# Kernel tuning notes

Measured on AMD Instinct MI355X. Metric: run time of the kernel, lower is better.

The kernel has to match this reference:

```python
import jax, jax.numpy as jnp
import numpy as np
from jax import lax

DN = ('NHWC', 'HWIO', 'NHWC')


def setup_inputs() -> dict:
    key = jax.random.key(0)
    k1, k2, k3, k4, k5, k6 = jax.random.split(key, 6)
    B = 1024
    vals = jax.random.normal(k1, (B, 64, 64, 1), dtype=jnp.float32)
    active = (jax.random.uniform(k2, (B, 64, 64, 1)) < 0.1).astype(jnp.float32)
    x = vals * active
    W1 = jax.random.normal(k3, (3, 3, 1, 64), dtype=jnp.float32) * 0.1
    b1 = jax.random.normal(k4, (64,), dtype=jnp.float32) * 0.1
    W2 = jax.random.normal(k5, (3, 3, 64, 32), dtype=jnp.float32) * 0.05
    b2 = jax.random.normal(k6, (32,), dtype=jnp.float32) * 0.05
    return {"x": x, "W1": W1, "b1": b1, "W2": W2, "b2": b2}


def reference(x, W1, b1, W2, b2):
    # x: [B, 64, 64, 1] NHWC (spconv from_dense layout); active sites = nonzero pixels
    m0 = (jnp.abs(x).max(axis=-1, keepdims=True) > 0).astype(x.dtype)  # [B,64,64,1]
    # SparseConv2d(1,64,3,stride=1, pad=0): output indices = any active input in 3x3 window
    m1 = lax.reduce_window(m0, jnp.array(0, x.dtype), lax.max,
                           (1, 3, 3, 1), (1, 1, 1, 1), 'VALID')  # [B,62,62,1]
    y = lax.conv_general_dilated(x, W1, (1, 1), 'VALID', dimension_numbers=DN)
    y = (y + b1) * m1  # bias only at active output sites; [B,62,62,64]
    # SparseInverseConv2d(64,32,3): transposed conv restricted to the ORIGINAL
    # active index set (indice_key='cp0'), i.e. output only where m0 is active.
    z = lax.conv_transpose(y, W2, (1, 1), 'VALID', dimension_numbers=DN)  # [B,64,64,32]
    z = (z + b2) * m0
    # SparseConvTensor.dense() returns NCHW
    return jnp.transpose(z, (0, 3, 1, 2))
```

## Files before the change

### kernel.cpp

```cpp
#include <hip/hip_runtime.h>

#define BDIM 256
#define KC_STRIDE 28
#define CASE_STRIDE (32 * KC_STRIDE)
#define SP 1032

typedef float floatx4 __attribute__((ext_vector_type(4)));

__device__ __forceinline__ int casef(int p) {
  return ((unsigned)(p - 2) < 60u) ? 2 : (p < 2 ? p : p - 59);
}

__global__ __launch_bounds__(BDIM) void prep_kernel(
    const float* __restrict__ W1, const float* __restrict__ b1,
    const float* __restrict__ W2, const float* __restrict__ b2,
    float* __restrict__ ws) {
  __shared__ float Mlds[9 * 9 * 32];
  __shared__ float BvL[9 * 32];
  const int tid = threadIdx.x;
  const int co = tid & 31;
  for (int tap = tid >> 5; tap < 9; tap += 8) {
    float acc[9] = {0.f, 0.f, 0.f, 0.f, 0.f, 0.f, 0.f, 0.f, 0.f};
    float accB = 0.f;
    for (int ci = 0; ci < 64; ++ci) {
      float w2 = W2[(tap * 64 + ci) * 32 + co];
      accB = fmaf(b1[ci], w2, accB);
#pragma unroll
      for (int e = 0; e < 9; ++e) acc[e] = fmaf(W1[e * 64 + ci], w2, acc[e]);
    }
#pragma unroll
    for (int e = 0; e < 9; ++e) Mlds[(tap * 9 + e) * 32 + co] = acc[e];
    BvL[tap * 32 + co] = accB;
  }
  __syncthreads();

  const int a = blockIdx.x / 5, c = blockIdx.x % 5;
  const int dmask[5] = {4, 6, 7, 3, 1};
  const int Da = dmask[a], Dc = dmask[c];
  for (int t = tid; t < CASE_STRIDE; t += BDIM) {
    int cc = t / KC_STRIDE, r = t % KC_STRIDE;
    float s = 0.f;
    if (r < 25) {
      int u = r / 5, v = r % 5;
      for (int di = 0; di < 3; ++di) {
        if (!((Da >> di) & 1)) continue;
        int ei = u - di;
        if ((unsigned)ei > 2u) continue;
        for (int dj = 0; dj < 3; ++dj) {
          if (!((Dc >> dj) & 1)) continue;
          int ej = v - dj;
          if ((unsigned)ej > 2u) continue;
          s += Mlds[((di * 3 + dj) * 9 + ei * 3 + ej) * 32 + cc];
        }
      }
    } else if (r == 25) {
      s = b2[cc];
      for (int di = 0; di < 3; ++di)
        if ((Da >> di) & 1)
          for (int dj = 0; dj < 3; ++dj)
            if ((Dc >> dj) & 1) s += BvL[(di * 3 + dj) * 32 + cc];
    }
    ws[blockIdx.x * CASE_STRIDE + t] = s;
  }
}

__global__ __launch_bounds__(BDIM) void main_kernel(
    const float* __restrict__ x, const float* __restrict__ ws,
    float* __restrict__ out) {
  const int bb = blockIdx.x;
  const int b = bb >> 1;
  const int r0 = (bb & 1) << 5;
  const int tid = threadIdx.x;
  const int lane = tid & 63;
  const int wave = tid >> 6;

  __shared__ __align__(16) float xp[36 * 68];
  __shared__ __align__(16) float S[8][SP];
  __shared__ __align__(16) float KiL[CASE_STRIDE];
  __shared__ unsigned long long Rm[32];
  __shared__ unsigned short aqi[2][224], aqb[2][64];
  __shared__ int nqi_sh[2], nqb_sh[2];

  if (tid < 2) { nqi_sh[tid] = 0; nqb_sh[tid] = 0; }
  float4* xp4 = reinterpret_cast<float4*>(xp);
  for (int i = tid; i < 612; i += BDIM) xp4[i] = make_float4(0.f, 0.f, 0.f, 0.f);
  for (int i = tid; i < CASE_STRIDE; i += BDIM) KiL[i] = ws[12 * CASE_STRIDE + i];
  __syncthreads();

  const float* xb = x + (size_t)b * 4096;
  for (int it = tid; it < 576; it += BDIM) {
    int i = it >> 4, c4 = (it & 15) << 2;
    int r = r0 - 2 + i;
    if ((unsigned)r < 64u) {
      float4 v = *reinterpret_cast<const float4*>(xb + r * 64 + c4);
      float2* d2 = reinterpret_cast<float2*>(&xp[i * 68 + 2 + c4]);
      d2[0] = make_float2(v.x, v.y);
      d2[1] = make_float2(v.z, v.w);
    }
  }
  __syncthreads();

  for (int k = wave; k < 32; k += 4) {
    int pred = (xp[(k + 2) * 68 + 2 + lane] != 0.0f);
    unsigned long long m = __ballot(pred);
    if (lane == 0) Rm[k] = m;
  }
  __syncthreads();

  for (int g = tid; g < 512; g += BDIM) {
    int k = g >> 4, q0 = (g & 15) << 2;
    unsigned bits = (unsigned)(Rm[k] >> q0) & 0xFu;
    if (!bits) continue;
    int h = k >> 4;
    int p = r0 + k;
    bool inter = ((unsigned)(p - 2) < 60u) && ((unsigned)(q0 - 4) <= 52u);
    if (inter) {
      aqi[h][atomicAdd(&nqi_sh[h], 1)] = (unsigned short)g;
    } else {
      aqb[h][atomicAdd(&nqb_sh[h], 1)] = (unsigned short)g;
    }
  }
  __syncthreads();

  const int ni0 = nqi_sh[0], ni1 = nqi_sh[1];
  const int nb0 = nqb_sh[0], nb1 = nqb_sh[1];
  float* outb = out + (size_t)b * (32 * 4096);

  for (int t = 0; t < 8; ++t) {
    const int cg = t >> 1, h = t & 1;
    const int ni = h ? ni1 : ni0;
    const int nb = h ? nb1 : nb0;
    for (int n = tid; n < ni * 4; n += BDIM) {
      int g = aqi[h][n >> 2];
      int co4 = n & 3;
      int co_lo = (cg << 3) + co4;
      int k = g >> 4, q0 = (g & 15) << 2;
      const float* Ka = &KiL[co_lo * KC_STRIDE];
      const float* Kb = &KiL[(co_lo + 4) * KC_STRIDE];
      float ba = Ka[25], bbv = Kb[25];
      float a0 = ba, a1 = ba, a2 = ba, a3 = ba;
      float b0 = bbv, b1 = bbv, b2 = bbv, b3 = bbv;
#pragma unroll
      for (int u = 0; u < 5; ++u) {
        const float* xr = &xp[(k + u) * 68 + q0];
        float4 xa = *reinterpret_cast<const float4*>(xr);
        float4 xc = *reinterpret_cast<const float4*>(xr + 4);
        float xv[8] = {xa.x, xa.y, xa.z, xa.w, xc.x, xc.y, xc.z, xc.w};
#pragma unroll
        for (int v = 0; v < 5; ++v) {
          float ka = Ka[u * 5 + v], kb = Kb[u * 5 + v];
          a0 = fmaf(xv[v], ka, a0);
          a1 = fmaf(xv[v + 1], ka, a1);
          a2 = fmaf(xv[v + 2], ka, a2);
          a3 = fmaf(xv[v + 3], ka, a3);
          b0 = fmaf(xv[v], kb, b0);
          b1 = fmaf(xv[v + 1], kb, b1);
          b2 = fmaf(xv[v + 2], kb, b2);
          b3 = fmaf(xv[v + 3], kb, b3);
        }
      }
      int so = ((k & 15) << 6) + q0;
      *reinterpret_cast<float4*>(&S[co4][so]) = make_float4(a0, a1, a2, a3);
      *reinterpret_cast<float4*>(&S[co4 + 4][so]) = make_float4(b0, b1, b2, b3);
    }
    for (int n = tid; n < nb * 8; n += BDIM) {
      int g = aqb[h][n >> 3];
      int cs = n & 7;
      int co = (cg << 3) + cs;
      int k = g >> 4, q0 = (g & 15) << 2;
      int p = r0 + k;
      int cp = casef(p);
      const float* K0 = ws + ((cp * 5 + casef(q0)) * 32 + co) * KC_STRIDE;
      const float* K1 = ws + ((cp * 5 + casef(q0 + 1)) * 32 + co) * KC_STRIDE;
      const float* K2 = ws + ((cp * 5 + casef(q0 + 2)) * 32 + co) * KC_STRIDE;
      const float* K3 = ws + ((cp * 5 + casef(q0 + 3)) * 32 + co) * KC_STRIDE;
      float z0 = K0[25], z1 = K1[25], z2 = K2[25], z3 = K3[25];
#pragma unroll
      for (int u = 0; u < 5; ++u) {
        const float* xr = &xp[(k + u) * 68 + q0];
        float4 xa = *reinterpret_cast<const float4*>(xr);
        float4 xc = *reinterpret_cast<const float4*>(xr + 4);
        float xv[8] = {xa.x, xa.y, xa.z, xa.w, xc.x, xc.y, xc.z, xc.w};
#pragma unroll
        for (int v = 0; v < 5; ++v) {
          int o = u * 5 + v;
          z0 = fmaf(xv[v], K0[o], z0);
          z1 = fmaf(xv[v + 1], K1[o], z1);
          z2 = fmaf(xv[v + 2], K2[o], z2);
          z3 = fmaf(xv[v + 3], K3[o], z3);
        }
      }
      *reinterpret_cast<float4*>(&S[cs][((k & 15) << 6) + q0]) =
          make_float4(z0, z1, z2, z3);
    }
    asm volatile("s_waitcnt lgkmcnt(0)" ::: "memory");
    __builtin_amdgcn_s_barrier();
    {
      int co_a = (cg << 3) + wave;
      int co_b = co_a + 4;
      float* dstA = outb + (((size_t)co_a) << 12) + ((r0 + (h << 4)) << 6);
      float* dstB = outb + (((size_t)co_b) << 12) + ((r0 + (h << 4)) << 6);
      const floatx4* SpA = reinterpret_cast<const floatx4*>(&S[wave][0]);
      const floatx4* SpB = reinterpret_cast<const floatx4*>(&S[wave + 4][0]);
#pragma unroll
      for (int i = 0; i < 4; ++i) {
        int f4 = (i << 6) + lane;
        int kk = f4 >> 4, q0 = (f4 & 15) << 2;
        unsigned bits = (unsigned)(Rm[(h << 4) + kk] >> q0) & 0xFu;
        floatx4 va = SpA[f4];
        floatx4 vb = SpB[f4];
        if (!(bits & 1u)) { va.x = 0.f; vb.x = 0.f; }
        if (!(bits & 2u)) { va.y = 0.f; vb.y = 0.f; }
        if (!(bits & 4u)) { va.z = 0.f; vb.z = 0.f; }
        if (!(bits & 8u)) { va.w = 0.f; vb.w = 0.f; }
        __builtin_nontemporal_store(va, reinterpret_cast<floatx4*>(dstA + (f4 << 2)));
        __builtin_nontemporal_store(vb, reinterpret_cast<floatx4*>(dstB + (f4 << 2)));
      }
    }
    asm volatile("s_waitcnt lgkmcnt(0)" ::: "memory");
    __builtin_amdgcn_s_barrier();
  }
}

extern "C" void kernel_launch(void* const* d_in, const int* in_sizes, int n_in,
                              void* d_out, int out_size, void* d_ws, size_t ws_size,
                              hipStream_t stream) {
  const float* x  = (const float*)d_in[0];
  const float* W1 = (const float*)d_in[1];
  const float* b1 = (const float*)d_in[2];
  const float* W2 = (const float*)d_in[3];
  const float* b2 = (const float*)d_in[4];
  float* out = (float*)d_out;
  float* ws  = (float*)d_ws;
  int B = in_sizes[0] / 4096;

  hipLaunchKernelGGL(prep_kernel, dim3(25), dim3(BDIM), 0, stream, W1, b1, W2, b2, ws);
  hipLaunchKernelGGL(main_kernel, dim3(2 * B), dim3(BDIM), 0, stream, x, ws, out);
}
```

Measured before the change: 136.0 us.

## Compute border outputs as interior kernel minus row/column/corner corrections from LDS

Border pixel groups no longer read per-case fused 5x5 kernels from global memory. They start from the interior kernel held in LDS and subtract precomputed row and column correction terms, then add corner terms back, with all tables staged in shared memory. A 26th prep block writes these correction tables. The aim is to remove scattered global loads in the border path, at the cost of extra LDS per block (about 24KB), which may lower occupancy, and extra FMAs for border pixels.

```diff
diff --git a/kernel.cpp b/kernel.cpp
--- a/kernel.cpp
+++ b/kernel.cpp
@@ -4,6 +4,13 @@
 #define KC_STRIDE 28
 #define CASE_STRIDE (32 * KC_STRIDE)
 #define SP 1032
+
+#define OFF_M 22400
+#define OFF_MR 24992
+#define OFF_MC 26432
+#define OFF_BVR 27872
+#define OFF_BVC 27968
+#define OFF_BV 28064
 
 typedef float floatx4 __attribute__((ext_vector_type(4)));
 
@@ -34,35 +41,93 @@
   }
   __syncthreads();
 
-  const int a = blockIdx.x / 5, c = blockIdx.x % 5;
-  const int dmask[5] = {4, 6, 7, 3, 1};
-  const int Da = dmask[a], Dc = dmask[c];
-  for (int t = tid; t < CASE_STRIDE; t += BDIM) {
-    int cc = t / KC_STRIDE, r = t % KC_STRIDE;
-    float s = 0.f;
-    if (r < 25) {
-      int u = r / 5, v = r % 5;
+  if (blockIdx.x < 25) {
+    const int a = blockIdx.x / 5, c = blockIdx.x % 5;
+    const int dmask[5] = {4, 6, 7, 3, 1};
+    const int Da = dmask[a], Dc = dmask[c];
+    for (int t = tid; t < CASE_STRIDE; t += BDIM) {
+      int cc = t / KC_STRIDE, r = t % KC_STRIDE;
+      float s = 0.f;
+      if (r < 25) {
+        int u = r / 5, v = r % 5;
+        for (int di = 0; di < 3; ++di) {
+          if (!((Da >> di) & 1)) continue;
+          int ei = u - di;
+          if ((unsigned)ei > 2u) continue;
+          for (int dj = 0; dj < 3; ++dj) {
+            if (!((Dc >> dj) & 1)) continue;
+            int ej = v - dj;
+            if ((unsigned)ej > 2u) continue;
+            s += Mlds[((di * 3 + dj) * 9 + ei * 3 + ej) * 32 + cc];
+          }
+        }
+      } else if (r == 25) {
+        s = b2[cc];
+        for (int di = 0; di < 3; ++di)
+          if ((Da >> di) & 1)
+            for (int dj = 0; dj < 3; ++dj)
+              if ((Dc >> dj) & 1) s += BvL[(di * 3 + dj) * 32 + cc];
+      }
+      ws[blockIdx.x * CASE_STRIDE + t] = s;
+    }
+  } else {
+    for (int t = tid; t < 2592; t += BDIM) ws[OFF_M + t] = Mlds[t];
+    for (int t = tid; t < 1440; t += BDIM) {
+      int di = t / 480, r = (t / 32) % 15, cc = t & 31;
+      int ei = r / 5, v = r % 5;
+      float s = 0.f;
+      for (int dj = 0; dj < 3; ++dj) {
+        int ej = v - dj;
+        if ((unsigned)ej <= 2u) s += Mlds[((di * 3 + dj) * 9 + ei * 3 + ej) * 32 + cc];
+      }
+      ws[OFF_MR + t] = s;
+    }
+    for (int t = tid; t < 1440; t += BDIM) {
+      int dj = t / 480, r = (t / 32) % 15, cc = t & 31;
+      int u = r / 3, ej = r % 3;
+      float s = 0.f;
       for (int di = 0; di < 3; ++di) {
-        if (!((Da >> di) & 1)) continue;
         int ei = u - di;
-        if ((unsigned)ei > 2u) continue;
-        for (int dj = 0; dj < 3; ++dj) {
-          if (!((Dc >> dj) & 1)) continue;
-          int ej = v - dj;
-          if ((unsigned)ej > 2u) continue;
-          s += Mlds[((di * 3 + dj) * 9 + ei * 3 + ej) * 32 + cc];
-        }
-      }
-    } else if (r == 25) {
-      s = b2[cc];
-      for (int di = 0; di < 3; ++di)
-        if ((Da >> di) & 1)
-          for (int dj = 0; dj < 3; ++dj)
-            if ((Dc >> dj) & 1) s += BvL[(di * 3 + dj) * 32 + cc];
-    }
-    ws[blockIdx.x * CASE_STRIDE + t] = s;
+        if ((unsigned)ei <= 2u) s += Mlds[((di * 3 + dj) * 9 + ei * 3 + ej) * 32 + cc];
+      }
+      ws[OFF_MC + t] = s;
+    }
+    for (int t = tid; t < 96; t += BDIM) {
+      int di = t >> 5, cc = t & 31;
+      float s = 0.f;
+      for (int dj = 0; dj < 3; ++dj) s += BvL[(di * 3 + dj) * 32 + cc];
+      ws[OFF_BVR + t] = s;
+    }
+    for (int t = tid; t < 96; t += BDIM) {
+      int dj = t >> 5, cc = t & 31;
+      float s = 0.f;
+      for (int di = 0; di < 3; ++di) s += BvL[(di * 3 + dj) * 32 + cc];
+      ws[OFF_BVC + t] = s;
+    }
+    for (int t = tid; t < 288; t += BDIM) ws[OFF_BV + t] = BvL[t];
   }
 }
+
+#define ROWCORR(DI)                                                            \
+  { float bv = BvRl[(DI)*32 + co]; z0 -= bv; z1 -= bv; z2 -= bv; z3 -= bv;     \
+    _Pragma("unroll") for (int ei = 0; ei < 3; ++ei)                           \
+    _Pragma("unroll") for (int v = 0; v < 5; ++v) {                            \
+      float m = MRl[((DI)*15 + ei*5 + v)*32 + co];                             \
+      z0 = fmaf(-xw[(DI)+ei][v], m, z0);   z1 = fmaf(-xw[(DI)+ei][v+1], m, z1);\
+      z2 = fmaf(-xw[(DI)+ei][v+2], m, z2); z3 = fmaf(-xw[(DI)+ei][v+3], m, z3);} }
+
+#define COLCORR(DJ, J, Z)                                                      \
+  { Z -= BvCl[(DJ)*32 + co];                                                   \
+    _Pragma("unroll") for (int u = 0; u < 5; ++u)                              \
+    _Pragma("unroll") for (int ej = 0; ej < 3; ++ej)                           \
+      Z = fmaf(-xw[u][(DJ)+ej+(J)], MCl[((DJ)*15 + u*3 + ej)*32 + co], Z); }
+
+#define CORNER(DI, DJ, J, Z)                                                   \
+  { Z += Bvl[((DI)*3+(DJ))*32 + co];                                           \
+    _Pragma("unroll") for (int ei = 0; ei < 3; ++ei)                           \
+    _Pragma("unroll") for (int ej = 0; ej < 3; ++ej)                           \
+      Z = fmaf(xw[(DI)+ei][(DJ)+ej+(J)],                                       \
+               Ml[(((DI)*3+(DJ))*9 + ei*3 + ej)*32 + co], Z); }
 
 __global__ __launch_bounds__(BDIM) void main_kernel(
     const float* __restrict__ x, const float* __restrict__ ws,
@@ -77,6 +142,8 @@
   __shared__ __align__(16) float xp[36 * 68];
   __shared__ __align__(16) float S[8][SP];
   __shared__ __align__(16) float KiL[CASE_STRIDE];
+  __shared__ float Ml[2592], MRl[1440], MCl[1440];
+  __shared__ float BvRl[96], BvCl[96], Bvl[288];
   __shared__ unsigned long long Rm[32];
   __shared__ unsigned short aqi[2][224], aqb[2][64];
   __shared__ int nqi_sh[2], nqb_sh[2];
@@ -85,6 +152,10 @@
   float4* xp4 = reinterpret_cast<float4*>(xp);
   for (int i = tid; i < 612; i += BDIM) xp4[i] = make_float4(0.f, 0.f, 0.f, 0.f);
   for (int i = tid; i < CASE_STRIDE; i += BDIM) KiL[i] = ws[12 * CASE_STRIDE + i];
+  for (int i = tid; i < 2592; i += BDIM) Ml[i] = ws[OFF_M + i];
+  for (int i = tid; i < 1440; i += BDIM) { MRl[i] = ws[OFF_MR + i]; MCl[i] = ws[OFF_MC + i]; }
+  if (tid < 96) { BvRl[tid] = ws[OFF_BVR + tid]; BvCl[tid] = ws[OFF_BVC + tid]; }
+  for (int i = tid; i < 288; i += BDIM) Bvl[i] = ws[OFF_BV + i];
   __syncthreads();
 
   const float* xb = x + (size_t)b * 4096;
@@ -169,26 +240,49 @@
       int co = (cg << 3) + cs;
       int k = g >> 4, q0 = (g & 15) << 2;
       int p = r0 + k;
-      int cp = casef(p);
-      const float* K0 = ws + ((cp * 5 + casef(q0)) * 32 + co) * KC_STRIDE;
-      const float* K1 = ws + ((cp * 5 + casef(q0 + 1)) * 32 + co) * KC_STRIDE;
-      const float* K2 = ws + ((cp * 5 + casef(q0 + 2)) * 32 + co) * KC_STRIDE;
-      const float* K3 = ws + ((cp * 5 + casef(q0 + 3)) * 32 + co) * KC_STRIDE;
-      float z0 = K0[25], z1 = K1[25], z2 = K2[25], z3 = K3[25];
+      float xw[5][8];
 #pragma unroll
       for (int u = 0; u < 5; ++u) {
         const float* xr = &xp[(k + u) * 68 + q0];
         float4 xa = *reinterpret_cast<const float4*>(xr);
         float4 xc = *reinterpret_cast<const float4*>(xr + 4);
-        float xv[8] = {xa.x, xa.y, xa.z, xa.w, xc.x, xc.y, xc.z, xc.w};
+        xw[u][0] = xa.x; xw[u][1] = xa.y; xw[u][2] = xa.z; xw[u][3] = xa.w;
+        xw[u][4] = xc.x; xw[u][5] = xc.y; xw[u][6] = xc.z; xw[u][7] = xc.w;
+      }
+      const float* Ki = &KiL[co * KC_STRIDE];
+      float bias = Ki[25];
+      float z0 = bias, z1 = bias, z2 = bias, z3 = bias;
+#pragma unroll
+      for (int u = 0; u < 5; ++u) {
 #pragma unroll
         for (int v = 0; v < 5; ++v) {
-          int o = u * 5 + v;
-          z0 = fmaf(xv[v], K0[o], z0);
-          z1 = fmaf(xv[v + 1], K1[o], z1);
-          z2 = fmaf(xv[v + 2], K2[o], z2);
-          z3 = fmaf(xv[v + 3], K3[o], z3);
+          float kv = Ki[u * 5 + v];
+          z0 = fmaf(xw[u][v], kv, z0);
+          z1 = fmaf(xw[u][v + 1], kv, z1);
+          z2 = fmaf(xw[u][v + 2], kv, z2);
+          z3 = fmaf(xw[u][v + 3], kv, z3);
         }
+      }
+      if (p == 0)       { ROWCORR(0) ROWCORR(1) }
+      else if (p == 1)  { ROWCORR(0) }
+      else if (p == 62) { ROWCORR(2) }
+      else if (p == 63) { ROWCORR(1) ROWCORR(2) }
+      if (q0 == 0) {
+        COLCORR(0, 0, z0) COLCORR(1, 0, z0) COLCORR(0, 1, z1)
+        if (p == 0)       { CORNER(0,0,0,z0) CORNER(0,1,0,z0) CORNER(0,0,1,z1)
+                            CORNER(1,0,0,z0) CORNER(1,1,0,z0) CORNER(1,0,1,z1) }
+        else if (p == 1)  { CORNER(0,0,0,z0) CORNER(0,1,0,z0) CORNER(0,0,1,z1) }
+        else if (p == 62) { CORNER(2,0,0,z0) CORNER(2,1,0,z0) CORNER(2,0,1,z1) }
+        else if (p == 63) { CORNER(1,0,0,z0) CORNER(1,1,0,z0) CORNER(1,0,1,z1)
+                            CORNER(2,0,0,z0) CORNER(2,1,0,z0) CORNER(2,0,1,z1) }
+      } else if (q0 == 60) {
+        COLCORR(2, 2, z2) COLCORR(1, 3, z3) COLCORR(2, 3, z3)
+        if (p == 0)       { CORNER(0,2,2,z2) CORNER(0,1,3,z3) CORNER(0,2,3,z3)
+                            CORNER(1,2,2,z2) CORNER(1,1,3,z3) CORNER(1,2,3,z3) }
+        else if (p == 1)  { CORNER(0,2,2,z2) CORNER(0,1,3,z3) CORNER(0,2,3,z3) }
+        else if (p == 62) { CORNER(2,2,2,z2) CORNER(2,1,3,z3) CORNER(2,2,3,z3) }
+        else if (p == 63) { CORNER(1,2,2,z2) CORNER(1,1,3,z3) CORNER(1,2,3,z3)
+                            CORNER(2,2,2,z2) CORNER(2,1,3,z3) CORNER(2,2,3,z3) }
       }
       *reinterpret_cast<float4*>(&S[cs][((k & 15) << 6) + q0]) =
           make_float4(z0, z1, z2, z3);
@@ -197,9 +291,8 @@
     __builtin_amdgcn_s_barrier();
     {
       int co_a = (cg << 3) + wave;
-      int co_b = co_a + 4;
       float* dstA = outb + (((size_t)co_a) << 12) + ((r0 + (h << 4)) << 6);
-      float* dstB = outb + (((size_t)co_b) << 12) + ((r0 + (h << 4)) << 6);
+      float* dstB = outb + (((size_t)(co_a + 4)) << 12) + ((r0 + (h << 4)) << 6);
       const floatx4* SpA = reinterpret_cast<const floatx4*>(&S[wave][0]);
       const floatx4* SpB = reinterpret_cast<const floatx4*>(&S[wave + 4][0]);
 #pragma unroll
@@ -234,6 +327,6 @@
   float* ws  = (float*)d_ws;
   int B = in_sizes[0] / 4096;
 
-  hipLaunchKernelGGL(prep_kernel, dim3(25), dim3(BDIM), 0, stream, W1, b1, W2, b2, ws);
+  hipLaunchKernelGGL(prep_kernel, dim3(26), dim3(BDIM), 0, stream, W1, b1, W2, b2, ws);
   hipLaunchKernelGGL(main_kernel, dim3(2 * B), dim3(BDIM), 0, stream, x, ws, out);
 }
```

Result: slower. 164.7 us (+21.2%).

## Process full 32-row tile per channel group and hold interior weights in registers

Applied to the files above, without the earlier changes.

The staging buffer S is doubled so each channel group handles all 32 rows at once, halving the outer loop from 8 to 4 iterations and cutting barrier count. The interior kernel weights are now loaded from global memory into per-thread register arrays once per channel group instead of being read from a shared-memory copy. This removes the LDS copy of the weights and the per-FMA LDS weight reads, at the cost of higher register pressure and nearly double the shared memory for S, which may reduce occupancy.

```diff
diff --git a/kernel.cpp b/kernel.cpp
--- a/kernel.cpp
+++ b/kernel.cpp
@@ -3,7 +3,7 @@
 #define BDIM 256
 #define KC_STRIDE 28
 #define CASE_STRIDE (32 * KC_STRIDE)
-#define SP 1032
+#define SP 2052
 
 typedef float floatx4 __attribute__((ext_vector_type(4)));
 
@@ -76,15 +76,13 @@
 
   __shared__ __align__(16) float xp[36 * 68];
   __shared__ __align__(16) float S[8][SP];
-  __shared__ __align__(16) float KiL[CASE_STRIDE];
   __shared__ unsigned long long Rm[32];
-  __shared__ unsigned short aqi[2][224], aqb[2][64];
-  __shared__ int nqi_sh[2], nqb_sh[2];
-
-  if (tid < 2) { nqi_sh[tid] = 0; nqb_sh[tid] = 0; }
+  __shared__ unsigned short aqi[448], aqb[128];
+  __shared__ int nqi_sh, nqb_sh;
+
+  if (tid == 0) { nqi_sh = 0; nqb_sh = 0; }
   float4* xp4 = reinterpret_cast<float4*>(xp);
   for (int i = tid; i < 612; i += BDIM) xp4[i] = make_float4(0.f, 0.f, 0.f, 0.f);
-  for (int i = tid; i < CASE_STRIDE; i += BDIM) KiL[i] = ws[12 * CASE_STRIDE + i];
   __syncthreads();
 
   const float* xb = x + (size_t)b * 4096;
@@ -111,33 +109,34 @@
     int k = g >> 4, q0 = (g & 15) << 2;
     unsigned bits = (unsigned)(Rm[k] >> q0) & 0xFu;
     if (!bits) continue;
-    int h = k >> 4;
     int p = r0 + k;
     bool inter = ((unsigned)(p - 2) < 60u) && ((unsigned)(q0 - 4) <= 52u);
     if (inter) {
-      aqi[h][atomicAdd(&nqi_sh[h], 1)] = (unsigned short)g;
+      aqi[atomicAdd(&nqi_sh, 1)] = (unsigned short)g;
     } else {
-      aqb[h][atomicAdd(&nqb_sh[h], 1)] = (unsigned short)g;
-    }
-  }
-  __syncthreads();
-
-  const int ni0 = nqi_sh[0], ni1 = nqi_sh[1];
-  const int nb0 = nqb_sh[0], nb1 = nqb_sh[1];
+      aqb[atomicAdd(&nqb_sh, 1)] = (unsigned short)g;
+    }
+  }
+  __syncthreads();
+
+  const int nqi = nqi_sh, nqb = nqb_sh;
   float* outb = out + (size_t)b * (32 * 4096);
-
-  for (int t = 0; t < 8; ++t) {
-    const int cg = t >> 1, h = t & 1;
-    const int ni = h ? ni1 : ni0;
-    const int nb = h ? nb1 : nb0;
-    for (int n = tid; n < ni * 4; n += BDIM) {
-      int g = aqi[h][n >> 2];
-      int co4 = n & 3;
-      int co_lo = (cg << 3) + co4;
+  const float* wsKi = ws + 12 * CASE_STRIDE;
+  const int co4 = tid & 3;
+
+  for (int cg = 0; cg < 4; ++cg) {
+    const int co_lo = (cg << 3) + co4;
+    float KA[26], KB[26];
+    {
+      const float* KpA = wsKi + co_lo * KC_STRIDE;
+      const float* KpB = wsKi + (co_lo + 4) * KC_STRIDE;
+#pragma unroll
+      for (int j = 0; j < 26; ++j) { KA[j] = KpA[j]; KB[j] = KpB[j]; }
+    }
+    for (int n = tid; n < nqi * 4; n += BDIM) {
+      int g = aqi[n >> 2];
       int k = g >> 4, q0 = (g & 15) << 2;
-      const float* Ka = &KiL[co_lo * KC_STRIDE];
-      const float* Kb = &KiL[(co_lo + 4) * KC_STRIDE];
-      float ba = Ka[25], bbv = Kb[25];
+      float ba = KA[25], bbv = KB[25];
       float a0 = ba, a1 = ba, a2 = ba, a3 = ba;
       float b0 = bbv, b1 = bbv, b2 = bbv, b3 = bbv;
 #pragma unroll
@@ -148,7 +147,7 @@
         float xv[8] = {xa.x, xa.y, xa.z, xa.w, xc.x, xc.y, xc.z, xc.w};
 #pragma unroll
         for (int v = 0; v < 5; ++v) {
-          float ka = Ka[u * 5 + v], kb = Kb[u * 5 + v];
+          float ka = KA[u * 5 + v], kb = KB[u * 5 + v];
           a0 = fmaf(xv[v], ka, a0);
           a1 = fmaf(xv[v + 1], ka, a1);
           a2 = fmaf(xv[v + 2], ka, a2);
@@ -159,12 +158,12 @@
           b3 = fmaf(xv[v + 3], kb, b3);
         }
       }
-      int so = ((k & 15) << 6) + q0;
+      int so = (k << 6) + q0;
       *reinterpret_cast<float4*>(&S[co4][so]) = make_float4(a0, a1, a2, a3);
       *reinterpret_cast<float4*>(&S[co4 + 4][so]) = make_float4(b0, b1, b2, b3);
     }
-    for (int n = tid; n < nb * 8; n += BDIM) {
-      int g = aqb[h][n >> 3];
+    for (int n = tid; n < nqb * 8; n += BDIM) {
+      int g = aqb[n >> 3];
       int cs = n & 7;
       int co = (cg << 3) + cs;
       int k = g >> 4, q0 = (g & 15) << 2;
@@ -190,23 +189,22 @@
           z3 = fmaf(xv[v + 3], K3[o], z3);
         }
       }
-      *reinterpret_cast<float4*>(&S[cs][((k & 15) << 6) + q0]) =
+      *reinterpret_cast<float4*>(&S[cs][(k << 6) + q0]) =
           make_float4(z0, z1, z2, z3);
     }
     asm volatile("s_waitcnt lgkmcnt(0)" ::: "memory");
     __builtin_amdgcn_s_barrier();
     {
       int co_a = (cg << 3) + wave;
-      int co_b = co_a + 4;
-      float* dstA = outb + (((size_t)co_a) << 12) + ((r0 + (h << 4)) << 6);
-      float* dstB = outb + (((size_t)co_b) << 12) + ((r0 + (h << 4)) << 6);
+      float* dstA = outb + (((size_t)co_a) << 12) + (r0 << 6);
+      float* dstB = outb + (((size_t)(co_a + 4)) << 12) + (r0 << 6);
       const floatx4* SpA = reinterpret_cast<const floatx4*>(&S[wave][0]);
       const floatx4* SpB = reinterpret_cast<const floatx4*>(&S[wave + 4][0]);
 #pragma unroll
-      for (int i = 0; i < 4; ++i) {
+      for (int i = 0; i < 8; ++i) {
         int f4 = (i << 6) + lane;
         int kk = f4 >> 4, q0 = (f4 & 15) << 2;
-        unsigned bits = (unsigned)(Rm[(h << 4) + kk] >> q0) & 0xFu;
+        unsigned bits = (unsigned)(Rm[kk] >> q0) & 0xFu;
         floatx4 va = SpA[f4];
         floatx4 vb = SpB[f4];
         if (!(bits & 1u)) { va.x = 0.f; vb.x = 0.f; }
```

Measured after the change: 124.8 us. 1.09x faster.
